# Performance work log

Hardware: AMD Instinct MI355X
Metric: run time of the kernel (lower is better)

The kernel has to match this reference:

```python
import jax, jax.numpy as jnp
import numpy as np

N, E, C = 65536, 1_048_576, 128
DEPTH, RATIO = 3, 0.5
N_CONVS = 2 * DEPTH  # 3 down + 2 up + 1 final


def setup_inputs() -> dict:
    key = jax.random.key(0)
    k1, k2, k3, k4 = jax.random.split(key, 4)
    x = jax.random.normal(k1, (N, C), jnp.float32)
    edge_index = jax.random.randint(k2, (2, E), 0, N, dtype=jnp.int32)
    Wl = jax.random.normal(k3, (N_CONVS, C, C), jnp.float32) * 0.05  # neighbor weights
    Wr = jax.random.normal(k4, (N_CONVS, C, C), jnp.float32) * 0.05  # root weights
    b = jnp.zeros((N_CONVS, C), jnp.float32)
    return {"x": x, "edge_index": edge_index, "Wl": Wl, "Wr": Wr, "b": b}


def sage_conv(x, src, dst, mask, Wl, Wr, b):
    # mean-aggregate SAGEConv: W_l * mean_{j->i} x_j + W_r * x_i + b
    n = x.shape[0]
    w = mask.astype(x.dtype)
    agg = jax.ops.segment_sum(x[src] * w[:, None], dst, num_segments=n)
    deg = jax.ops.segment_sum(w, dst, num_segments=n)
    mean = agg / jnp.maximum(deg, 1.0)[:, None]
    return mean @ Wl + x @ Wr + b


def diff_pool(x, src, dst, mask, k):
    # top-k pooling: score by feature norm, keep k nodes, gate by tanh(score),
    # relabel edges; dropped edges kept (static shape) but masked out.
    score = jnp.sqrt(jnp.sum(x * x, axis=-1) + 1e-12)
    vals, perm = jax.lax.top_k(score, k)
    xp = x[perm] * jnp.tanh(vals)[:, None]
    n = x.shape[0]
    mapping = jnp.full((n,), -1, src.dtype).at[perm].set(jnp.arange(k, dtype=src.dtype))
    ns, nd = mapping[src], mapping[dst]
    nm = mask & (ns >= 0) & (nd >= 0)
    return xp, jnp.where(nm, ns, 0), jnp.where(nm, nd, 0), nm, perm


def forward(x, src, dst, Wl, Wr, b):
    xs = [x]
    srcs, dsts, masks = [src], [dst], [jnp.ones(src.shape, bool)]
    perms = []
    L = jnp.zeros((), x.dtype)
    n = x.shape[0]
    # ---- down path: pool -> conv -> relu, with per-level losses ----
    for i in range(DEPTH):
        k = int(np.ceil(RATIO * n))
        xp, s, d, m, perm = diff_pool(xs[-1], srcs[-1], dsts[-1], masks[-1], k)
        h = jax.nn.relu(sage_conv(xp, s, d, m, Wl[i], Wr[i], b[i]))
        if i < DEPTH - 1:
            k2 = int(np.ceil(RATIO * k))
            nx, _, _, _, p2 = diff_pool(h, s, d, m, k2)
            L = L + jnp.mean((h[p2] - nx) ** 2)          # L_FP (fixed point)
        L = L + jnp.mean((h - xs[0][perm]) ** 2)          # L_similarity
        L = L + jnp.mean(jnp.abs(h - xs[-1][perm]))       # L_regularization
        xs.append(h)
        srcs.append(s); dsts.append(d); masks.append(m); perms.append(perm)
        n = k
    # ---- up path: scatter-unpool -> conv -> relu ----
    h = xs[-1]
    for i in range(DEPTH - 1, 0, -1):
        up = jnp.zeros((xs[i].shape[0], h.shape[1]), h.dtype).at[perms[i]].set(h)
        ci = DEPTH + i - 1  # convs[4] then convs[3]
        h = jax.nn.relu(sage_conv(up, srcs[i], dsts[i], masks[i], Wl[ci], Wr[ci], b[ci]))
    up0 = jnp.zeros((xs[0].shape[0], h.shape[1]), h.dtype).at[perms[0]].set(h)
    out = sage_conv(up0, srcs[0], dsts[0], masks[0], Wl[-1], Wr[-1], b[-1])
    return out, L


def reference(x, edge_index, Wl, Wr, b):
    src, dst = edge_index[0], edge_index[1]
    return forward(x, src, dst, Wl, Wr, b)
```

## Files before the change

kernel.cpp:

```cpp
#include <hip/hip_runtime.h>
#include <math.h>

typedef unsigned int uint;
typedef unsigned long long u64;

#define C_ 128
static const int N0 = 65536;
static const int E0 = 1048576;
static const int K0 = 32768, K1 = 16384, K2 = 8192;
static const int CAP1 = 524288, CAP2 = 262144, CAP3 = 131072;

__device__ inline float wave_reduce_sum(float v) {
#pragma unroll
  for (int w = 32; w >= 1; w >>= 1) v += __shfl_xor(v, w, 64);
  return v;
}

__global__ void score_kernel(const float* __restrict__ x, float* __restrict__ score,
                             float* __restrict__ ss) {
  int row = blockIdx.x * 4 + (threadIdx.x >> 6);
  int lane = threadIdx.x & 63;
  float2 v = ((const float2*)(x + (size_t)row * C_))[lane];
  float s = v.x * v.x + v.y * v.y;
  s = wave_reduce_sum(s);
  if (lane == 0) { ss[row] = s; score[row] = sqrtf(s + 1e-12f); }
}

__global__ __launch_bounds__(1024) void select_kernel(const float* __restrict__ score, int n,
                                                      int k, uint* __restrict__ kth_out,
                                                      int* __restrict__ map) {
  const uint* keys = (const uint*)score;
  const uint4* keys4 = (const uint4*)score;
  __shared__ int hist[256];
  __shared__ uint s_kth;
  __shared__ int s_rem;
  __shared__ int eqlist[2048];
  __shared__ int eqn;
  int tid = threadIdx.x;
  int lane = tid & 63;
  int n4 = n >> 2;
  if (tid == 0) { s_rem = k; s_kth = 0u; eqn = 0; }
  __syncthreads();
  for (int pass = 3; pass >= 0; --pass) {
    int sh = pass * 8;
    if (tid < 256) hist[tid] = 0;
    __syncthreads();
    uint prefix = s_kth;
    uint maskhi = (pass == 3) ? 0u : (0xFFFFFFFFu << (sh + 8));
    for (int i = tid; i < n4; i += 1024) {
      uint4 v4 = keys4[i];
#pragma unroll
      for (int c = 0; c < 4; ++c) {
        uint v = (c == 0) ? v4.x : (c == 1) ? v4.y : (c == 2) ? v4.z : v4.w;
        bool valid = (v & maskhi) == prefix;
        u64 m = __ballot(valid);
        if (!m) continue;
        uint b = (v >> sh) & 255u;
#pragma unroll
        for (int bit = 0; bit < 8; ++bit) {
          u64 bb = __ballot((b >> bit) & 1u);
          m &= ((b >> bit) & 1u) ? bb : ~bb;
        }
        if (valid) {
          int leader = __ffsll(m) - 1;
          if (lane == leader) atomicAdd(&hist[b], (int)__popcll(m));
        }
      }
    }
    __syncthreads();
    if (tid == 0) {
      int rem = s_rem;
      int b = 255;
      for (;; --b) { int c = hist[b]; if (c >= rem) break; rem -= c; }
      s_rem = rem;
      s_kth = prefix | ((uint)b << sh);
    }
    __syncthreads();
  }
  uint kth = s_kth;
  for (int i = tid; i < n; i += 1024) {
    if (keys[i] == kth) { int p = atomicAdd(&eqn, 1); if (p < 2048) eqlist[p] = i; }
  }
  __syncthreads();
  if (tid == 0) {
    int need = s_rem;
    int tot = eqn < 2048 ? eqn : 2048;
    for (int t = 0; t < need && t < tot; ++t) {
      int mi = -1, mv = 0x7FFFFFFF;
      for (int q = 0; q < tot; ++q) { int v = eqlist[q]; if (v >= 0 && v < mv) { mv = v; mi = q; } }
      if (mi < 0) break;
      map[mv] = -2;
      eqlist[mi] = -1;
    }
    *kth_out = kth;
  }
}

__global__ __launch_bounds__(256) void build_perm_kernel(
    const float* __restrict__ score, const float* __restrict__ ss,
    const uint* __restrict__ kth_ptr, int* __restrict__ map, int* __restrict__ perm,
    float* __restrict__ gate, int* __restrict__ ctr, float lfp_scale,
    float* __restrict__ Lacc) {
  const int ITER = 4;
  int tid = threadIdx.x, lane = tid & 63, wid = tid >> 6;
  __shared__ int wbase[4];
  __shared__ int gbase;
  __shared__ float pl[4];
  uint kth = *kth_ptr;
  int base = blockIdx.x * (256 * ITER);
  int cnt = 0;
#pragma unroll
  for (int l = 0; l < ITER; ++l) {
    int i = base + l * 256 + tid;
    uint key = ((const uint*)score)[i];
    if ((key > kth) || (map[i] == -2)) ++cnt;
  }
#pragma unroll
  for (int w = 32; w >= 1; w >>= 1) cnt += __shfl_xor(cnt, w, 64);
  if (lane == 0) wbase[wid] = cnt;
  __syncthreads();
  if (tid == 0) {
    int s = 0;
#pragma unroll
    for (int i = 0; i < 4; ++i) { int c = wbase[i]; wbase[i] = s; s += c; }
    gbase = s ? atomicAdd(ctr, s) : 0;
  }
  __syncthreads();
  int woff = gbase + wbase[wid];
  float lfp = 0.f;
#pragma unroll
  for (int l = 0; l < ITER; ++l) {
    int i = base + l * 256 + tid;
    uint key = ((const uint*)score)[i];
    bool sel = (key > kth) || (map[i] == -2);
    u64 m = __ballot(sel);
    if (sel) {
      int j = woff + (int)__popcll(m & ((1ull << lane) - 1ull));
      perm[j] = i;
      map[i] = j;
      float t = tanhf(score[i]);
      gate[j] = t;
      if (lfp_scale != 0.f) { float om = 1.f - t; lfp += om * om * ss[i] * lfp_scale; }
    }
    woff += (int)__popcll(m);
  }
  if (lfp_scale != 0.f) {
    lfp = wave_reduce_sum(lfp);
    if (lane == 0) pl[wid] = lfp;
    __syncthreads();
    if (tid == 0) atomicAdd(Lacc, pl[0] + pl[1] + pl[2] + pl[3]);
  }
}

__global__ void pool_gather_kernel(const float* __restrict__ xin, const int* __restrict__ perm,
                                   const float* __restrict__ gate, float* __restrict__ xp) {
  int t = blockIdx.x * 256 + threadIdx.x;
  int j = t >> 5, q = t & 31;
  int p = perm[j];
  float g = gate[j];
  float4 v = ((const float4*)(xin + (size_t)p * C_))[q];
  v.x *= g; v.y *= g; v.z *= g; v.w *= g;
  ((float4*)(xp + (size_t)j * C_))[q] = v;
}

__global__ __launch_bounds__(256) void edge_compact_kernel(
    const int* __restrict__ src, const int* __restrict__ dst,
    const int* __restrict__ cnt_ptr, int in_cap, const int* __restrict__ map,
    int* __restrict__ osrc, int* __restrict__ odst, int* __restrict__ octr, int cap,
    int* __restrict__ deg) {
  const int ITER = 8;
  int n = cnt_ptr ? min(*cnt_ptr, in_cap) : in_cap;
  int tid = threadIdx.x, lane = tid & 63, wid = tid >> 6;
  __shared__ int wbase[4];
  __shared__ int gbase;
  long long chunk = 256 * ITER;
  for (long long base = (long long)blockIdx.x * chunk; base < n;
       base += (long long)gridDim.x * chunk) {
    int cnt = 0;
#pragma unroll
    for (int l = 0; l < ITER; ++l) {
      long long e = base + l * 256 + tid;
      if (e < n) {
        int a = map[src[e]];
        int b = map[dst[e]];
        if (a >= 0 && b >= 0) ++cnt;
      }
    }
#pragma unroll
    for (int w = 32; w >= 1; w >>= 1) cnt += __shfl_xor(cnt, w, 64);
    __syncthreads();
    if (lane == 0) wbase[wid] = cnt;
    __syncthreads();
    if (tid == 0) {
      int s = 0;
#pragma unroll
      for (int i = 0; i < 4; ++i) { int c = wbase[i]; wbase[i] = s; s += c; }
      gbase = s ? atomicAdd(octr, s) : 0;
    }
    __syncthreads();
    int woff = gbase + wbase[wid];
#pragma unroll
    for (int l = 0; l < ITER; ++l) {
      long long e = base + l * 256 + tid;
      int a = -1, b = -1;
      bool keep = false;
      if (e < n) {
        a = map[src[e]];
        b = map[dst[e]];
        keep = (a >= 0 && b >= 0);
      }
      u64 m = __ballot(keep);
      if (keep) {
        int p = woff + (int)__popcll(m & ((1ull << lane) - 1ull));
        if (p < cap) {
          osrc[p] = a;
          odst[p] = b;
          atomicAdd(&deg[b], 1);
        }
      }
      woff += (int)__popcll(m);
    }
  }
}

__global__ void hist_kernel(const int* __restrict__ dst, int n, int* __restrict__ deg) {
  for (int e = blockIdx.x * 256 + threadIdx.x; e < n; e += gridDim.x * 256)
    atomicAdd(&deg[dst[e]], 1);
}

__global__ __launch_bounds__(1024) void scan_kernel(int* __restrict__ cursor,
                                                    int* __restrict__ rowptr, int n) {
  __shared__ int part[1024];
  int tid = threadIdx.x;
  int chunk = (n + 1023) >> 10;
  int beg = tid * chunk, end = min(beg + chunk, n);
  int s = 0;
  for (int i = beg; i < end; ++i) s += cursor[i];
  part[tid] = s;
  __syncthreads();
  for (int d = 1; d < 1024; d <<= 1) {
    int v = part[tid];
    if (tid >= d) v += part[tid - d];
    __syncthreads();
    part[tid] = v;
    __syncthreads();
  }
  int off = part[tid] - s;
  for (int i = beg; i < end; ++i) { int dv = cursor[i]; rowptr[i] = off; cursor[i] = off; off += dv; }
  if (tid == 1023) rowptr[n] = part[1023];
}

__global__ void scatter_kernel(const int* __restrict__ src, const int* __restrict__ dst,
                               const int* __restrict__ cnt_ptr, int cap,
                               int* __restrict__ cursor, int* __restrict__ csr) {
  int n = cnt_ptr ? min(*cnt_ptr, cap) : cap;
  for (int e = blockIdx.x * 256 + threadIdx.x; e < n; e += gridDim.x * 256) {
    int p = atomicAdd(&cursor[dst[e]], 1);
    csr[p] = src[e];
  }
}

__global__ void agg_kernel(const float* __restrict__ x, const int* __restrict__ rowptr,
                           const int* __restrict__ csr, const int* __restrict__ fmap,
                           float* __restrict__ mean, int n) {
  int t = blockIdx.x * 256 + threadIdx.x;
  int node = t >> 5, q = t & 31;
  if (node >= n) return;
  int beg = rowptr[node], end = rowptr[node + 1];
  float4 acc = make_float4(0.f, 0.f, 0.f, 0.f);
  if (fmap) {
    for (int p = beg; p < end; ++p) {
      int m = fmap[csr[p]];
      if (m < 0) continue;
      float4 v = ((const float4*)(x + (size_t)m * C_))[q];
      acc.x += v.x; acc.y += v.y; acc.z += v.z; acc.w += v.w;
    }
  } else {
    for (int p = beg; p < end; ++p) {
      int s = csr[p];
      float4 v = ((const float4*)(x + (size_t)s * C_))[q];
      acc.x += v.x; acc.y += v.y; acc.z += v.z; acc.w += v.w;
    }
  }
  float inv = 1.f / fmaxf((float)(end - beg), 1.f);
  acc.x *= inv; acc.y *= inv; acc.z *= inv; acc.w *= inv;
  ((float4*)(mean + (size_t)node * C_))[q] = acc;
}

__global__ __launch_bounds__(256) void gemm_kernel(const float* __restrict__ Amean,
                                                   const float* __restrict__ Xsrc,
                                                   const int* __restrict__ xmask,
                                                   const float* __restrict__ Wl,
                                                   const float* __restrict__ Wr,
                                                   const float* __restrict__ bias,
                                                   float* __restrict__ out, int relu,
                                                   float* __restrict__ Lout,
                                                   const float* __restrict__ Lacc) {
  __shared__ alignas(16) float As[32][68];
  __shared__ alignas(16) float Ws[32][128];
  __shared__ int rm[64];
  int tid = threadIdx.x;
  int row0 = blockIdx.x * 64;
  if (tid < 64) rm[tid] = xmask ? xmask[row0 + tid] : (row0 + tid);
  if (Lout && blockIdx.x == 0 && tid == 0) Lout[0] = *Lacc;
  int trow = tid >> 4;
  int tcol = tid & 15;
  float acc[4][8];
#pragma unroll
  for (int i = 0; i < 4; ++i)
#pragma unroll
    for (int j = 0; j < 8; ++j) acc[i][j] = 0.f;
  __syncthreads();
  for (int phase = 0; phase < 2; ++phase) {
    const float* A = phase ? Xsrc : Amean;
    const float* W = phase ? Wr : Wl;
    for (int kc = 0; kc < 128; kc += 32) {
#pragma unroll
      for (int l = 0; l < 2; ++l) {
        int f = tid + l * 256;
        int r = f >> 3, c4 = (f & 7) << 2;
        int xr = phase ? rm[r] : (row0 + r);
        float4 v = make_float4(0.f, 0.f, 0.f, 0.f);
        if (xr >= 0) v = *(const float4*)(A + (size_t)xr * C_ + kc + c4);
        As[c4 + 0][r] = v.x; As[c4 + 1][r] = v.y; As[c4 + 2][r] = v.z; As[c4 + 3][r] = v.w;
      }
#pragma unroll
      for (int l = 0; l < 4; ++l) {
        int f = tid + l * 256;
        int kk = f >> 5, c4 = (f & 31) << 2;
        *(float4*)(&Ws[kk][c4]) = *(const float4*)(W + (size_t)(kc + kk) * C_ + c4);
      }
      __syncthreads();
#pragma unroll
      for (int kk = 0; kk < 32; ++kk) {
        float a[4], w[8];
#pragma unroll
        for (int i = 0; i < 4; ++i) a[i] = As[kk][trow * 4 + i];
#pragma unroll
        for (int j = 0; j < 8; ++j) w[j] = Ws[kk][tcol * 8 + j];
#pragma unroll
        for (int i = 0; i < 4; ++i)
#pragma unroll
          for (int j = 0; j < 8; ++j) acc[i][j] = fmaf(a[i], w[j], acc[i][j]);
      }
      __syncthreads();
    }
  }
#pragma unroll
  for (int i = 0; i < 4; ++i) {
    int r = row0 + trow * 4 + i;
#pragma unroll
    for (int j = 0; j < 8; ++j) {
      float v = acc[i][j] + bias[tcol * 8 + j];
      if (relu) v = fmaxf(v, 0.f);
      out[(size_t)r * C_ + tcol * 8 + j] = v;
    }
  }
}

__global__ void lsim_score_kernel(const float* __restrict__ h, const float* __restrict__ x0,
                                  const float* __restrict__ xin, const int* __restrict__ perm,
                                  float scale, float* __restrict__ Lacc,
                                  float* __restrict__ score, float* __restrict__ ss) {
  int row = blockIdx.x * 4 + (threadIdx.x >> 6);
  int lane = threadIdx.x & 63;
  int p = perm[row];
  float2 hv = ((const float2*)(h + (size_t)row * C_))[lane];
  float2 a = ((const float2*)(x0 + (size_t)p * C_))[lane];
  float2 bv = (xin == x0) ? a : ((const float2*)(xin + (size_t)p * C_))[lane];
  float d1x = hv.x - a.x, d1y = hv.y - a.y;
  float l = d1x * d1x + d1y * d1y + fabsf(hv.x - bv.x) + fabsf(hv.y - bv.y);
  float s2 = hv.x * hv.x + hv.y * hv.y;
#pragma unroll
  for (int w = 32; w >= 1; w >>= 1) { l += __shfl_xor(l, w, 64); s2 += __shfl_xor(s2, w, 64); }
  __shared__ float pl[4];
  int wid = threadIdx.x >> 6;
  if (lane == 0) {
    pl[wid] = l;
    if (score) { ss[row] = s2; score[row] = sqrtf(s2 + 1e-12f); }
  }
  __syncthreads();
  if (threadIdx.x == 0) atomicAdd(Lacc, (pl[0] + pl[1] + pl[2] + pl[3]) * scale);
}

extern "C" void kernel_launch(void* const* d_in, const int* in_sizes, int n_in, void* d_out,
                              int out_size, void* d_ws, size_t ws_size, hipStream_t stream) {
  const float* x0 = (const float*)d_in[0];
  const int* ei = (const int*)d_in[1];
  const float* Wl = (const float*)d_in[2];
  const float* Wr = (const float*)d_in[3];
  const float* bias = (const float*)d_in[4];
  float* out = (float*)d_out;

  char* base = (char*)d_ws;
  size_t off = 0;
  auto alloc = [&](size_t bytes) -> char* {
    char* p = base + off;
    off = (off + bytes + 255) & ~(size_t)255;
    return p;
  };

  int* ctrl = (int*)alloc(1024 * 4);
  int* cur0 = (int*)alloc((size_t)(N0 + 1) * 4);
  int* cur1 = (int*)alloc((size_t)(K0 + 1) * 4);
  int* cur2 = (int*)alloc((size_t)(K1 + 1) * 4);
  int* cur3 = (int*)alloc((size_t)(K2 + 1) * 4);
  size_t zero_bytes = (size_t)((base + off) - (char*)ctrl);
  int* map0 = (int*)alloc((size_t)N0 * 4);
  int* map1 = (int*)alloc((size_t)K0 * 4);
  int* map2 = (int*)alloc((size_t)K1 * 4);
  size_t ff_bytes = (size_t)((base + off) - (char*)map0);
  float* score0 = (float*)alloc((size_t)N0 * 4);
  float* ss0 = (float*)alloc((size_t)N0 * 4);
  float* score1 = (float*)alloc((size_t)K0 * 4);
  float* ss1 = (float*)alloc((size_t)K0 * 4);
  float* score2 = (float*)alloc((size_t)K1 * 4);
  float* ss2 = (float*)alloc((size_t)K1 * 4);
  int* perm0 = (int*)alloc((size_t)K0 * 4);
  int* perm1 = (int*)alloc((size_t)K1 * 4);
  int* perm2 = (int*)alloc((size_t)K2 * 4);
  float* gate0 = (float*)alloc((size_t)K0 * 4);
  float* gate1 = (float*)alloc((size_t)K1 * 4);
  float* gate2 = (float*)alloc((size_t)K2 * 4);
  int* e1s = (int*)alloc((size_t)CAP1 * 4);
  int* e1d = (int*)alloc((size_t)CAP1 * 4);
  int* e2s = (int*)alloc((size_t)CAP2 * 4);
  int* e2d = (int*)alloc((size_t)CAP2 * 4);
  int* e3s = (int*)alloc((size_t)CAP3 * 4);
  int* e3d = (int*)alloc((size_t)CAP3 * 4);
  int* rowptr0 = (int*)alloc((size_t)(N0 + 1) * 4);
  int* rowptr1 = (int*)alloc((size_t)(K0 + 1) * 4);
  int* rowptr2 = (int*)alloc((size_t)(K1 + 1) * 4);
  int* rowptr3 = (int*)alloc((size_t)(K2 + 1) * 4);
  int* csr0 = (int*)alloc((size_t)E0 * 4);
  int* csr1 = (int*)alloc((size_t)CAP1 * 4);
  int* csr2 = (int*)alloc((size_t)CAP2 * 4);
  int* csr3 = (int*)alloc((size_t)CAP3 * 4);
  float* xp = (float*)alloc((size_t)K0 * C_ * 4);
  float* h0 = (float*)alloc((size_t)K0 * C_ * 4);
  float* h1 = (float*)alloc((size_t)K1 * C_ * 4);
  float* h2 = (float*)alloc((size_t)K2 * C_ * 4);
  float* mean = (float*)alloc((size_t)N0 * C_ * 4);

  uint* kth0 = (uint*)(ctrl + 8);
  uint* kth1 = (uint*)(ctrl + 9);
  uint* kth2 = (uint*)(ctrl + 10);
  float* Lacc = (float*)(ctrl + 16);
  const float sc0 = 1.f / ((float)K0 * C_);
  const float sc1 = 1.f / ((float)K1 * C_);
  const float sc2 = 1.f / ((float)K2 * C_);

  hipMemsetAsync(ctrl, 0, zero_bytes, stream);
  hipMemsetAsync(map0, 0xFF, ff_bytes, stream);

  hist_kernel<<<2048, 256, 0, stream>>>(ei + E0, E0, cur0);
  scan_kernel<<<1, 1024, 0, stream>>>(cur0, rowptr0, N0);
  scatter_kernel<<<2048, 256, 0, stream>>>(ei, ei + E0, nullptr, E0, cur0, csr0);

  score_kernel<<<N0 / 4, 256, 0, stream>>>(x0, score0, ss0);
  select_kernel<<<1, 1024, 0, stream>>>(score0, N0, K0, kth0, map0);
  build_perm_kernel<<<N0 / 1024, 256, 0, stream>>>(score0, ss0, kth0, map0, perm0, gate0,
                                                   ctrl + 4, 0.f, Lacc);
  pool_gather_kernel<<<K0 / 8, 256, 0, stream>>>(x0, perm0, gate0, xp);
  edge_compact_kernel<<<512, 256, 0, stream>>>(ei, ei + E0, nullptr, E0, map0, e1s, e1d,
                                               ctrl + 0, CAP1, cur1);
  scan_kernel<<<1, 1024, 0, stream>>>(cur1, rowptr1, K0);
  scatter_kernel<<<1024, 256, 0, stream>>>(e1s, e1d, ctrl + 0, CAP1, cur1, csr1);
  agg_kernel<<<K0 / 8, 256, 0, stream>>>(xp, rowptr1, csr1, nullptr, mean, K0);
  gemm_kernel<<<K0 / 64, 256, 0, stream>>>(mean, xp, nullptr, Wl, Wr, bias, h0, 1, nullptr, Lacc);
  lsim_score_kernel<<<K0 / 4, 256, 0, stream>>>(h0, x0, x0, perm0, sc0, Lacc, score1, ss1);

  select_kernel<<<1, 1024, 0, stream>>>(score1, K0, K1, kth1, map1);
  build_perm_kernel<<<K0 / 1024, 256, 0, stream>>>(score1, ss1, kth1, map1, perm1, gate1,
                                                   ctrl + 5, sc1, Lacc);
  pool_gather_kernel<<<K1 / 8, 256, 0, stream>>>(h0, perm1, gate1, xp);
  edge_compact_kernel<<<256, 256, 0, stream>>>(e1s, e1d, ctrl + 0, CAP1, map1, e2s, e2d,
                                               ctrl + 1, CAP2, cur2);
  scan_kernel<<<1, 1024, 0, stream>>>(cur2, rowptr2, K1);
  scatter_kernel<<<512, 256, 0, stream>>>(e2s, e2d, ctrl + 1, CAP2, cur2, csr2);
  agg_kernel<<<K1 / 8, 256, 0, stream>>>(xp, rowptr2, csr2, nullptr, mean, K1);
  gemm_kernel<<<K1 / 64, 256, 0, stream>>>(mean, xp, nullptr, Wl + 16384, Wr + 16384, bias + 128,
                                           h1, 1, nullptr, Lacc);
  lsim_score_kernel<<<K1 / 4, 256, 0, stream>>>(h1, x0, h0, perm1, sc1, Lacc, score2, ss2);

  select_kernel<<<1, 1024, 0, stream>>>(score2, K1, K2, kth2, map2);
  build_perm_kernel<<<K1 / 1024, 256, 0, stream>>>(score2, ss2, kth2, map2, perm2, gate2,
                                                   ctrl + 6, sc2, Lacc);
  pool_gather_kernel<<<K2 / 8, 256, 0, stream>>>(h1, perm2, gate2, xp);
  edge_compact_kernel<<<128, 256, 0, stream>>>(e2s, e2d, ctrl + 1, CAP2, map2, e3s, e3d,
                                               ctrl + 2, CAP3, cur3);
  scan_kernel<<<1, 1024, 0, stream>>>(cur3, rowptr3, K2);
  scatter_kernel<<<256, 256, 0, stream>>>(e3s, e3d, ctrl + 2, CAP3, cur3, csr3);
  agg_kernel<<<K2 / 8, 256, 0, stream>>>(xp, rowptr3, csr3, nullptr, mean, K2);
  gemm_kernel<<<K2 / 64, 256, 0, stream>>>(mean, xp, nullptr, Wl + 2 * 16384, Wr + 2 * 16384,
                                           bias + 256, h2, 1, nullptr, Lacc);
  lsim_score_kernel<<<K2 / 4, 256, 0, stream>>>(h2, x0, h1, perm2, sc2, Lacc, nullptr, nullptr);

  agg_kernel<<<K1 / 8, 256, 0, stream>>>(h2, rowptr2, csr2, map2, mean, K1);
  gemm_kernel<<<K1 / 64, 256, 0, stream>>>(mean, h2, map2, Wl + 4 * 16384, Wr + 4 * 16384,
                                           bias + 512, xp, 1, nullptr, Lacc);
  agg_kernel<<<K0 / 8, 256, 0, stream>>>(xp, rowptr1, csr1, map1, mean, K0);
  gemm_kernel<<<K0 / 64, 256, 0, stream>>>(mean, xp, map1, Wl + 3 * 16384, Wr + 3 * 16384,
                                           bias + 384, h0, 1, nullptr, Lacc);
  agg_kernel<<<N0 / 8, 256, 0, stream>>>(h0, rowptr0, csr0, map0, mean, N0);
  gemm_kernel<<<N0 / 64, 256, 0, stream>>>(mean, h0, map0, Wl + 5 * 16384, Wr + 5 * 16384,
                                           bias + 640, out, 0, out + (size_t)N0 * C_, Lacc);
}
```

Before: 1.410 ms.

## Split single-block top-k radix select into multi-block two-pass 16-bit histogram kernels

Replaces the single-workgroup 4-pass 8-bit radix select with a grid-wide two-pass 16-bit radix select. Global-atomic histogram kernels run across many blocks, a single-block scan picks the bucket, and separate kernels collect and resolve ties. This removes the serial bottleneck of one 1024-thread block scanning the scores four times. In exchange it adds six launches per pooling level, global atomic contention on a 65536-bin histogram, and extra zeroed workspace.

```diff
diff --git a/kernel.cpp b/kernel.cpp
--- a/kernel.cpp
+++ b/kernel.cpp
@@ -26,73 +26,81 @@
   if (lane == 0) { ss[row] = s; score[row] = sqrtf(s + 1e-12f); }
 }
 
-__global__ __launch_bounds__(1024) void select_kernel(const float* __restrict__ score, int n,
-                                                      int k, uint* __restrict__ kth_out,
-                                                      int* __restrict__ map) {
-  const uint* keys = (const uint*)score;
-  const uint4* keys4 = (const uint4*)score;
-  __shared__ int hist[256];
-  __shared__ uint s_kth;
-  __shared__ int s_rem;
-  __shared__ int eqlist[2048];
-  __shared__ int eqn;
+
+__global__ void hist_hi_kernel(const float* __restrict__ score, int n,
+                               int* __restrict__ hist) {
+  int i = blockIdx.x * 256 + threadIdx.x;
+  if (i < n) atomicAdd(&hist[((const uint*)score)[i] >> 16], 1);
+}
+
+__global__ void hist_lo_kernel(const float* __restrict__ score, int n,
+                               const uint* __restrict__ kth_ptr, int* __restrict__ hist) {
+  uint pre = *kth_ptr >> 16;
+  int i = blockIdx.x * 256 + threadIdx.x;
+  if (i < n) {
+    uint key = ((const uint*)score)[i];
+    if ((key >> 16) == pre) atomicAdd(&hist[key & 0xFFFFu], 1);
+  }
+}
+
+__global__ __launch_bounds__(1024) void radix_scan_kernel(const int* __restrict__ hist,
+                                                          int k_init, int use_init,
+                                                          uint* __restrict__ kth,
+                                                          int* __restrict__ rem, int shift) {
+  __shared__ int part[1024];
+  __shared__ int chunkidx;
   int tid = threadIdx.x;
-  int lane = tid & 63;
-  int n4 = n >> 2;
-  if (tid == 0) { s_rem = k; s_kth = 0u; eqn = 0; }
-  __syncthreads();
-  for (int pass = 3; pass >= 0; --pass) {
-    int sh = pass * 8;
-    if (tid < 256) hist[tid] = 0;
-    __syncthreads();
-    uint prefix = s_kth;
-    uint maskhi = (pass == 3) ? 0u : (0xFFFFFFFFu << (sh + 8));
-    for (int i = tid; i < n4; i += 1024) {
-      uint4 v4 = keys4[i];
-#pragma unroll
-      for (int c = 0; c < 4; ++c) {
-        uint v = (c == 0) ? v4.x : (c == 1) ? v4.y : (c == 2) ? v4.z : v4.w;
-        bool valid = (v & maskhi) == prefix;
-        u64 m = __ballot(valid);
-        if (!m) continue;
-        uint b = (v >> sh) & 255u;
-#pragma unroll
-        for (int bit = 0; bit < 8; ++bit) {
-          u64 bb = __ballot((b >> bit) & 1u);
-          m &= ((b >> bit) & 1u) ? bb : ~bb;
-        }
-        if (valid) {
-          int leader = __ffsll(m) - 1;
-          if (lane == leader) atomicAdd(&hist[b], (int)__popcll(m));
-        }
-      }
-    }
-    __syncthreads();
-    if (tid == 0) {
-      int rem = s_rem;
-      int b = 255;
-      for (;; --b) { int c = hist[b]; if (c >= rem) break; rem -= c; }
-      s_rem = rem;
-      s_kth = prefix | ((uint)b << sh);
-    }
-    __syncthreads();
-  }
-  uint kth = s_kth;
-  for (int i = tid; i < n; i += 1024) {
-    if (keys[i] == kth) { int p = atomicAdd(&eqn, 1); if (p < 2048) eqlist[p] = i; }
-  }
-  __syncthreads();
+  int s = 0;
+  int base = tid * 64;
+  for (int j = 0; j < 64; ++j) s += hist[base + j];
+  part[tid] = s;
+  __syncthreads();
+  for (int d = 1; d < 1024; d <<= 1) {
+    int add = (tid + d < 1024) ? part[tid + d] : 0;
+    __syncthreads();
+    part[tid] += add;
+    __syncthreads();
+  }
+  int remv = use_init ? k_init : *rem;
   if (tid == 0) {
-    int need = s_rem;
-    int tot = eqn < 2048 ? eqn : 2048;
-    for (int t = 0; t < need && t < tot; ++t) {
-      int mi = -1, mv = 0x7FFFFFFF;
-      for (int q = 0; q < tot; ++q) { int v = eqlist[q]; if (v >= 0 && v < mv) { mv = v; mi = q; } }
-      if (mi < 0) break;
-      map[mv] = -2;
-      eqlist[mi] = -1;
-    }
-    *kth_out = kth;
+    int c = 1023;
+    while (c >= 0 && part[c] < remv) --c;
+    chunkidx = c;
+  }
+  __syncthreads();
+  if (tid == 0) {
+    int c = chunkidx;
+    int above = (c + 1 < 1024) ? part[c + 1] : 0;
+    int b = c * 64 + 63;
+    int acc = above;
+    for (;; --b) { acc += hist[b]; if (acc >= remv) break; }
+    *rem = remv - (acc - hist[b]);
+    *kth |= ((uint)b) << shift;
+  }
+}
+
+__global__ void tie_collect_kernel(const float* __restrict__ score, int n,
+                                   const uint* __restrict__ kth_ptr,
+                                   int* __restrict__ eqlist, int* __restrict__ eqn) {
+  uint kth = *kth_ptr;
+  int i = blockIdx.x * 256 + threadIdx.x;
+  if (i < n && ((const uint*)score)[i] == kth) {
+    int p = atomicAdd(eqn, 1);
+    if (p < 4096) eqlist[p] = i;
+  }
+}
+
+__global__ void tie_mark_kernel(int* __restrict__ eqlist, const int* __restrict__ eqn_ptr,
+                                const int* __restrict__ rem_ptr, int* __restrict__ map) {
+  if (threadIdx.x != 0) return;
+  int need = *rem_ptr;
+  int tot = min(*eqn_ptr, 4096);
+  for (int t = 0; t < need && t < tot; ++t) {
+    int mi = -1, mv = 0x7FFFFFFF;
+    for (int q = 0; q < tot; ++q) { int v = eqlist[q]; if (v >= 0 && v < mv) { mv = v; mi = q; } }
+    if (mi < 0) break;
+    map[mv] = -2;
+    eqlist[mi] = -1;
   }
 }
 
@@ -405,11 +413,20 @@
   int* cur1 = (int*)alloc((size_t)(K0 + 1) * 4);
   int* cur2 = (int*)alloc((size_t)(K1 + 1) * 4);
   int* cur3 = (int*)alloc((size_t)(K2 + 1) * 4);
+  int* hhi0 = (int*)alloc(65536 * 4);
+  int* hlo0 = (int*)alloc(65536 * 4);
+  int* hhi1 = (int*)alloc(65536 * 4);
+  int* hlo1 = (int*)alloc(65536 * 4);
+  int* hhi2 = (int*)alloc(65536 * 4);
+  int* hlo2 = (int*)alloc(65536 * 4);
   size_t zero_bytes = (size_t)((base + off) - (char*)ctrl);
   int* map0 = (int*)alloc((size_t)N0 * 4);
   int* map1 = (int*)alloc((size_t)K0 * 4);
   int* map2 = (int*)alloc((size_t)K1 * 4);
   size_t ff_bytes = (size_t)((base + off) - (char*)map0);
+  int* eql0 = (int*)alloc(4096 * 4);
+  int* eql1 = (int*)alloc(4096 * 4);
+  int* eql2 = (int*)alloc(4096 * 4);
   float* score0 = (float*)alloc((size_t)N0 * 4);
   float* ss0 = (float*)alloc((size_t)N0 * 4);
   float* score1 = (float*)alloc((size_t)K0 * 4);
@@ -445,7 +462,13 @@
   uint* kth0 = (uint*)(ctrl + 8);
   uint* kth1 = (uint*)(ctrl + 9);
   uint* kth2 = (uint*)(ctrl + 10);
+  int* rem0 = ctrl + 12;
+  int* rem1 = ctrl + 13;
+  int* rem2 = ctrl + 14;
   float* Lacc = (float*)(ctrl + 16);
+  int* eqn0 = ctrl + 20;
+  int* eqn1 = ctrl + 21;
+  int* eqn2 = ctrl + 22;
   const float sc0 = 1.f / ((float)K0 * C_);
   const float sc1 = 1.f / ((float)K1 * C_);
   const float sc2 = 1.f / ((float)K2 * C_);
@@ -458,7 +481,12 @@
   scatter_kernel<<<2048, 256, 0, stream>>>(ei, ei + E0, nullptr, E0, cur0, csr0);
 
   score_kernel<<<N0 / 4, 256, 0, stream>>>(x0, score0, ss0);
-  select_kernel<<<1, 1024, 0, stream>>>(score0, N0, K0, kth0, map0);
+  hist_hi_kernel<<<N0 / 256, 256, 0, stream>>>(score0, N0, hhi0);
+  radix_scan_kernel<<<1, 1024, 0, stream>>>(hhi0, K0, 1, kth0, rem0, 16);
+  hist_lo_kernel<<<N0 / 256, 256, 0, stream>>>(score0, N0, kth0, hlo0);
+  radix_scan_kernel<<<1, 1024, 0, stream>>>(hlo0, 0, 0, kth0, rem0, 0);
+  tie_collect_kernel<<<N0 / 256, 256, 0, stream>>>(score0, N0, kth0, eql0, eqn0);
+  tie_mark_kernel<<<1, 64, 0, stream>>>(eql0, eqn0, rem0, map0);
   build_perm_kernel<<<N0 / 1024, 256, 0, stream>>>(score0, ss0, kth0, map0, perm0, gate0,
                                                    ctrl + 4, 0.f, Lacc);
   pool_gather_kernel<<<K0 / 8, 256, 0, stream>>>(x0, perm0, gate0, xp);
@@ -470,7 +498,12 @@
   gemm_kernel<<<K0 / 64, 256, 0, stream>>>(mean, xp, nullptr, Wl, Wr, bias, h0, 1, nullptr, Lacc);
   lsim_score_kernel<<<K0 / 4, 256, 0, stream>>>(h0, x0, x0, perm0, sc0, Lacc, score1, ss1);
 
-  select_kernel<<<1, 1024, 0, stream>>>(score1, K0, K1, kth1, map1);
+  hist_hi_kernel<<<K0 / 256, 256, 0, stream>>>(score1, K0, hhi1);
+  radix_scan_kernel<<<1, 1024, 0, stream>>>(hhi1, K1, 1, kth1, rem1, 16);
+  hist_lo_kernel<<<K0 / 256, 256, 0, stream>>>(score1, K0, kth1, hlo1);
+  radix_scan_kernel<<<1, 1024, 0, stream>>>(hlo1, 0, 0, kth1, rem1, 0);
+  tie_collect_kernel<<<K0 / 256, 256, 0, stream>>>(score1, K0, kth1, eql1, eqn1);
+  tie_mark_kernel<<<1, 64, 0, stream>>>(eql1, eqn1, rem1, map1);
   build_perm_kernel<<<K0 / 1024, 256, 0, stream>>>(score1, ss1, kth1, map1, perm1, gate1,
                                                    ctrl + 5, sc1, Lacc);
   pool_gather_kernel<<<K1 / 8, 256, 0, stream>>>(h0, perm1, gate1, xp);
@@ -483,7 +516,12 @@
                                            h1, 1, nullptr, Lacc);
   lsim_score_kernel<<<K1 / 4, 256, 0, stream>>>(h1, x0, h0, perm1, sc1, Lacc, score2, ss2);
 
-  select_kernel<<<1, 1024, 0, stream>>>(score2, K1, K2, kth2, map2);
+  hist_hi_kernel<<<K1 / 256, 256, 0, stream>>>(score2, K1, hhi2);
+  radix_scan_kernel<<<1, 1024, 0, stream>>>(hhi2, K2, 1, kth2, rem2, 16);
+  hist_lo_kernel<<<K1 / 256, 256, 0, stream>>>(score2, K1, kth2, hlo2);
+  radix_scan_kernel<<<1, 1024, 0, stream>>>(hlo2, 0, 0, kth2, rem2, 0);
+  tie_collect_kernel<<<K1 / 256, 256, 0, stream>>>(score2, K1, kth2, eql2, eqn2);
+  tie_mark_kernel<<<1, 64, 0, stream>>>(eql2, eqn2, rem2, map2);
   build_perm_kernel<<<K1 / 1024, 256, 0, stream>>>(score2, ss2, kth2, map2, perm2, gate2,
                                                    ctrl + 6, sc2, Lacc);
   pool_gather_kernel<<<K2 / 8, 256, 0, stream>>>(h1, perm2, gate2, xp);
```

Measured after the change: 1.560 ms. +10.6%, slower.
